# Kernel tuning notes

Hardware: AMD Instinct MI355X
Metric: run time of the kernel (lower is better)

The kernel has to match this reference:

```python
import jax, jax.numpy as jnp
import numpy as np

T, H, E, K, I, S = 512, 1024, 32, 4, 512, 2048  # tokens, hidden, experts, top_k, moe_inter, shared_inter


def setup_inputs() -> dict:
    key = jax.random.key(0)
    ks = jax.random.split(key, 8)
    sc = 0.02
    return {
        "hidden_states": jax.random.normal(ks[0], (T, H), jnp.float32),
        "Wg": jax.random.normal(ks[1], (H, E + 1), jnp.float32) * sc,          # router gate + shared gate (merged)
        "W_gate": jax.random.normal(ks[2], (E, H, I), jnp.float32) * sc,        # per-expert gate proj
        "W_up": jax.random.normal(ks[3], (E, H, I), jnp.float32) * sc,          # per-expert up proj
        "W_down": jax.random.normal(ks[4], (E, I, H), jnp.float32) * sc,        # per-expert down proj
        "Ws_gate": jax.random.normal(ks[5], (H, S), jnp.float32) * sc,          # shared expert gate proj
        "Ws_up": jax.random.normal(ks[6], (H, S), jnp.float32) * sc,            # shared expert up proj
        "Ws_down": jax.random.normal(ks[7], (S, H), jnp.float32) * sc,          # shared expert down proj
    }


def reference(hidden_states, Wg, W_gate, W_up, W_down, Ws_gate, Ws_up, Ws_down):
    x = hidden_states  # [T, H]
    logits = x @ Wg                       # [T, E+1]
    router_logits = logits[:, :E]         # [T, E]
    shared_gate_logits = logits[:, E:]    # [T, 1]

    # top-k softmax routing with renormalization (renormalize=True)
    probs = jax.nn.softmax(router_logits, axis=-1)          # [T, E]
    topk_w, topk_idx = jax.lax.top_k(probs, K)               # [T, K]
    topk_w = topk_w / jnp.sum(topk_w, axis=-1, keepdims=True)
    combine = jnp.zeros((T, E), x.dtype).at[jnp.arange(T)[:, None], topk_idx].add(topk_w)  # [T, E]

    # routed experts: dense reference over all experts, combined by routing weights
    g = jnp.einsum("th,ehi->eti", x, W_gate)                 # [E, T, I]
    u = jnp.einsum("th,ehi->eti", x, W_up)                   # [E, T, I]
    h = jax.nn.silu(g) * u                                    # SiluAndMul
    y = jnp.einsum("eti,eih->eth", h, W_down)                # [E, T, H]
    routed = jnp.einsum("te,eth->th", combine, y)            # [T, H]

    # shared expert MLP + sigmoid shared-gate
    sh = (jax.nn.silu(x @ Ws_gate) * (x @ Ws_up)) @ Ws_down  # [T, H]
    shared = jax.nn.sigmoid(shared_gate_logits) * sh

    return shared + routed
```

## Files before the change

### kernel.cpp

```cpp
#include <hip/hip_runtime.h>
#include <hip/hip_bf16.h>

#define TT 512
#define HH 1024
#define EE 32
#define KK 4
#define II 512
#define SS 2048

using f32x4 = __attribute__((ext_vector_type(4))) float;
using s16x8 = __attribute__((ext_vector_type(8))) short;

__device__ __forceinline__ unsigned short f2bf(float f){
  unsigned int u = __builtin_bit_cast(unsigned int, f);
  u += 0x7fffu + ((u >> 16) & 1u);
  return (unsigned short)(u >> 16);
}

__global__ __launch_bounds__(64) void k_router(
    const float* __restrict__ x, const float* __restrict__ Wg,
    unsigned short* __restrict__ xb, int* __restrict__ topk_idx,
    float* __restrict__ topk_w, float* __restrict__ sig_gate){
  int t = blockIdx.x; int l = threadIdx.x;
  const float* xr = x + (size_t)t * HH;
  #pragma unroll
  for(int i=0;i<HH/64;i++){
    int h = l + 64*i;
    xb[(size_t)t*HH + h] = f2bf(xr[h]);
  }
  float acc0=0.f, acc1=0.f, acc2=0.f, acc3=0.f;
  if(l < EE+1){
    const float* wcol = Wg + l;
    for(int h=0; h<HH; h+=4){
      acc0 += xr[h]   * wcol[(size_t)h*(EE+1)];
      acc1 += xr[h+1] * wcol[(size_t)(h+1)*(EE+1)];
      acc2 += xr[h+2] * wcol[(size_t)(h+2)*(EE+1)];
      acc3 += xr[h+3] * wcol[(size_t)(h+3)*(EE+1)];
    }
  }
  __shared__ float lg[EE+1];
  if(l < EE+1) lg[l] = (acc0+acc1)+(acc2+acc3);
  __syncthreads();
  if(l == 0){
    float v[EE];
    #pragma unroll
    for(int i=0;i<EE;i++) v[i]=lg[i];
    int idx[KK]; float val[KK];
    #pragma unroll
    for(int k=0;k<KK;k++){
      float m=-1e30f; int mi=0;
      for(int i=0;i<EE;i++){ if(v[i]>m){ m=v[i]; mi=i; } }
      idx[k]=mi; val[k]=m; v[mi]=-1e30f;
    }
    float mx = val[0], s=0.f; float w[KK];
    #pragma unroll
    for(int k=0;k<KK;k++){ w[k]=__expf(val[k]-mx); s+=w[k]; }
    float inv = 1.f/s;
    #pragma unroll
    for(int k=0;k<KK;k++){ topk_idx[t*KK+k]=idx[k]; topk_w[t*KK+k]=w[k]*inv; }
    sig_gate[t] = 1.f/(1.f+__expf(-lg[EE]));
  }
}

__global__ __launch_bounds__(64) void k_build(
    const int* __restrict__ topk_idx, const float* __restrict__ topk_w,
    int* __restrict__ token_list, float* __restrict__ weight_list,
    int* __restrict__ counts){
  int e = blockIdx.x; int l = threadIdx.x;
  int cnt = 0;
  for(int c=0;c<TT;c+=64){
    int t = c + l;
    int kk = -1;
    #pragma unroll
    for(int k=0;k<KK;k++) if(topk_idx[t*KK+k]==e) kk=k;
    unsigned long long b = __ballot(kk>=0);
    int pre = __popcll(b & ((1ull<<l)-1ull));
    if(kk>=0){
      token_list[e*TT + cnt + pre] = t;
      weight_list[e*TT + cnt + pre] = topk_w[t*KK+kk];
    }
    cnt += __popcll(b);
  }
  if(l==0) counts[e]=cnt;
}

__device__ __forceinline__ void stB(unsigned short* B, int nb, int krow,
                                    float4 r0, float4 r1){
  const float* a = (const float*)&r0;
  const float* b = (const float*)&r1;
  #pragma unroll
  for(int j=0;j<4;j++){
    unsigned v = (unsigned)f2bf(a[j]) | ((unsigned)f2bf(b[j]) << 16);
    *reinterpret_cast<unsigned*>(B + (size_t)(nb+j)*40 + krow) = v;
  }
}

template<bool DUAL>
__device__ __forceinline__ void gemm64(
    const unsigned short* A0, bool va,
    const float* Gp, const float* Up, int ldb, int NK,
    f32x4* ag, f32x4* au,
    unsigned short* As, unsigned short* Bg, unsigned short* Bu, int tid){
  const int w = tid>>6, l = tid&63;
  const int ar = tid>>2, as_ = tid&3;
  const int krow = 2*(tid>>4), nb = 4*(tid&15);
  const int kt = l>>4, mm = l&15;
  uint4 av = va ? *reinterpret_cast<const uint4*>(A0) : make_uint4(0,0,0,0);
  float4 g0 = *reinterpret_cast<const float4*>(Gp + (size_t)krow*ldb);
  float4 g1 = *reinterpret_cast<const float4*>(Gp + (size_t)(krow+1)*ldb);
  float4 u0, u1;
  if(DUAL){
    u0 = *reinterpret_cast<const float4*>(Up + (size_t)krow*ldb);
    u1 = *reinterpret_cast<const float4*>(Up + (size_t)(krow+1)*ldb);
  }
  *reinterpret_cast<uint4*>(As + (size_t)ar*40 + as_*8) = av;
  stB(Bg, nb, krow, g0, g1);
  if(DUAL) stB(Bu, nb, krow, u0, u1);
  __syncthreads();
  for(int ks=0; ks<NK; ks++){
    const int cur = ks & 1;
    const bool more = (ks+1 < NK);
    if(more){
      av = va ? *reinterpret_cast<const uint4*>(A0 + (size_t)(ks+1)*32)
              : make_uint4(0,0,0,0);
      const float* gb = Gp + (size_t)(ks+1)*32*ldb;
      g0 = *reinterpret_cast<const float4*>(gb + (size_t)krow*ldb);
      g1 = *reinterpret_cast<const float4*>(gb + (size_t)(krow+1)*ldb);
      if(DUAL){
        const float* ub = Up + (size_t)(ks+1)*32*ldb;
        u0 = *reinterpret_cast<const float4*>(ub + (size_t)krow*ldb);
        u1 = *reinterpret_cast<const float4*>(ub + (size_t)(krow+1)*ldb);
      }
    }
    s16x8 bg_[4], bu_[4];
    #pragma unroll
    for(int c=0;c<4;c++){
      bg_[c] = *reinterpret_cast<const s16x8*>(Bg + ((size_t)cur*64 + c*16 + mm)*40 + kt*8);
      if(DUAL)
        bu_[c] = *reinterpret_cast<const s16x8*>(Bu + ((size_t)cur*64 + c*16 + mm)*40 + kt*8);
    }
    s16x8 af = *reinterpret_cast<const s16x8*>(As + ((size_t)cur*64 + w*16 + mm)*40 + kt*8);
    #pragma unroll
    for(int c=0;c<4;c++){
      ag[c] = __builtin_amdgcn_mfma_f32_16x16x32_bf16(af, bg_[c], ag[c], 0,0,0);
      if(DUAL)
        au[c] = __builtin_amdgcn_mfma_f32_16x16x32_bf16(af, bu_[c], au[c], 0,0,0);
    }
    if(more){
      const int nx = cur^1;
      *reinterpret_cast<uint4*>(As + ((size_t)nx*64 + ar)*40 + as_*8) = av;
      stB(Bg + (size_t)nx*64*40, nb, krow, g0, g1);
      if(DUAL) stB(Bu + (size_t)nx*64*40, nb, krow, u0, u1);
    }
    __syncthreads();
  }
}

__global__ __launch_bounds__(256) void k_gateup_all(
    const unsigned short* __restrict__ xb,
    const float* __restrict__ Wsg, const float* __restrict__ Wsu,
    unsigned short* __restrict__ Hs,
    const float* __restrict__ Wgate, const float* __restrict__ Wup,
    const int* __restrict__ token_list, const int* __restrict__ counts,
    unsigned short* __restrict__ hbuf){
  __shared__ unsigned short As[2*64*40];
  __shared__ unsigned short Bg[2*64*40];
  __shared__ unsigned short Bu[2*64*40];
  int tid = threadIdx.x, w = tid>>6, l = tid&63;
  int ar = tid>>2, as_ = tid&3, nb = 4*(tid&15);
  int bid = blockIdx.x;
  f32x4 zero = {0.f,0.f,0.f,0.f};
  const int NSH = (TT/64)*(SS/64);

  if(bid < NSH){
    int n0 = (bid & 31) * 64;
    int r0 = (bid >> 5) * 64;
    f32x4 ag[4]={zero,zero,zero,zero}, au[4]={zero,zero,zero,zero};
    const unsigned short* A0 = xb + (size_t)(r0+ar)*HH + as_*8;
    const float* Gp = Wsg + n0 + nb;
    const float* Up = Wsu + n0 + nb;
    gemm64<true>(A0, true, Gp, Up, SS, HH/32, ag, au, As, Bg, Bu, tid);
    int mm = l&15, rb = r0 + w*16 + (l>>4)*4;
    #pragma unroll
    for(int c=0;c<4;c++){
      #pragma unroll
      for(int j=0;j<4;j++){
        float g = ag[c][j], u = au[c][j];
        Hs[(size_t)(rb+j)*SS + n0 + c*16 + mm] = f2bf(g*u/(1.f+__expf(-g)));
      }
    }
  } else {
    int b = bid - NSH;
    int e = b >> 3;
    int i0 = (b & 7) * 64;
    int cnt = counts[e]; if(cnt == 0) return;
    int off = 0;
    for(int i=0;i<e;i++) off += counts[i];
    const float* Gp0 = Wgate + (size_t)e*HH*II + i0 + nb;
    const float* Up0 = Wup   + (size_t)e*HH*II + i0 + nb;
    for(int rt=0; rt*64<cnt; rt++){
      int nv = cnt - rt*64; if(nv > 64) nv = 64;
      const int* rows = token_list + e*TT + rt*64;
      int arow = (ar < nv) ? rows[ar] : 0;
      bool va = ar < nv;
      f32x4 ag[4]={zero,zero,zero,zero}, au[4]={zero,zero,zero,zero};
      const unsigned short* A0 = xb + (size_t)arow*HH + as_*8;
      gemm64<true>(A0, va, Gp0, Up0, II, HH/32, ag, au, As, Bg, Bu, tid);
      int mm = l&15, rr0 = w*16 + (l>>4)*4;
      #pragma unroll
      for(int c=0;c<4;c++){
        #pragma unroll
        for(int j=0;j<4;j++){
          int rr = rr0 + j;
          if(rr < nv){
            float g = ag[c][j], u = au[c][j];
            hbuf[(size_t)(off+rt*64+rr)*II + i0 + c*16 + mm] =
                f2bf(g*u/(1.f+__expf(-g)));
          }
        }
      }
    }
  }
}

__global__ __launch_bounds__(256) void k_down_all(
    const unsigned short* __restrict__ Hsrc, const float* __restrict__ Wsd,
    const float* __restrict__ sig_gate,
    const unsigned short* __restrict__ hbuf, const float* __restrict__ Wdown,
    const int* __restrict__ token_list, const float* __restrict__ weight_list,
    const int* __restrict__ counts, float* __restrict__ out){
  __shared__ unsigned short As[2*64*40];
  __shared__ unsigned short Bs[2*64*40];
  int tid = threadIdx.x, w = tid>>6, l = tid&63;
  int ar = tid>>2, as_ = tid&3, nb = 4*(tid&15);
  int bid = blockIdx.x;
  f32x4 zero = {0.f,0.f,0.f,0.f};
  const int NSH = (TT/64)*(HH/64);

  if(bid < NSH){
    int n0 = (bid & 15) * 64;
    int r0 = (bid >> 4) * 64;
    f32x4 acc[4]={zero,zero,zero,zero};
    const unsigned short* A0 = Hsrc + (size_t)(r0+ar)*SS + as_*8;
    const float* Bp = Wsd + n0 + nb;
    gemm64<false>(A0, true, Bp, Bp, HH, SS/32, acc, acc, As, Bs, Bs, tid);
    int mm = l&15, rb = r0 + w*16 + (l>>4)*4;
    #pragma unroll
    for(int c=0;c<4;c++){
      #pragma unroll
      for(int j=0;j<4;j++){
        atomicAdd(&out[(size_t)(rb+j)*HH + n0 + c*16 + mm],
                  sig_gate[rb+j]*acc[c][j]);
      }
    }
  } else {
    int b = bid - NSH;
    int e = b >> 4;
    int n0 = (b & 15) * 64;
    int cnt = counts[e]; if(cnt == 0) return;
    int off = 0;
    for(int i=0;i<e;i++) off += counts[i];
    const float* Bp = Wdown + (size_t)e*II*HH + n0 + nb;
    for(int rt=0; rt*64<cnt; rt++){
      int nv = cnt - rt*64; if(nv > 64) nv = 64;
      bool va = ar < nv;
      f32x4 acc[4]={zero,zero,zero,zero};
      const unsigned short* A0 = hbuf + (size_t)(off+rt*64+ar)*II + as_*8;
      gemm64<false>(A0, va, Bp, Bp, HH, II/32, acc, acc, As, Bs, Bs, tid);
      int mm = l&15, rr0 = w*16 + (l>>4)*4;
      #pragma unroll
      for(int c=0;c<4;c++){
        #pragma unroll
        for(int j=0;j<4;j++){
          int rr = rr0 + j;
          if(rr < nv){
            int t = token_list[e*TT + rt*64 + rr];
            float wt = weight_list[e*TT + rt*64 + rr];
            atomicAdd(&out[(size_t)t*HH + n0 + c*16 + mm], wt*acc[c][j]);
          }
        }
      }
    }
  }
}

extern "C" void kernel_launch(void* const* d_in, const int* in_sizes, int n_in,
                              void* d_out, int out_size, void* d_ws, size_t ws_size,
                              hipStream_t stream) {
  const float* x     = (const float*)d_in[0];
  const float* Wg    = (const float*)d_in[1];
  const float* Wgate = (const float*)d_in[2];
  const float* Wup   = (const float*)d_in[3];
  const float* Wdown = (const float*)d_in[4];
  const float* Wsg   = (const float*)d_in[5];
  const float* Wsu   = (const float*)d_in[6];
  const float* Wsd   = (const float*)d_in[7];
  float* out = (float*)d_out;

  char* ws = (char*)d_ws;
  unsigned short* xb   = (unsigned short*)ws; ws += (size_t)TT*HH*2;
  unsigned short* Hs   = (unsigned short*)ws; ws += (size_t)TT*SS*2;
  unsigned short* hbuf = (unsigned short*)ws; ws += (size_t)(TT*KK+64)*II*2;
  int*   token_list  = (int*)ws;   ws += (size_t)EE*TT*4;
  float* weight_list = (float*)ws; ws += (size_t)EE*TT*4;
  int*   topk_idx    = (int*)ws;   ws += (size_t)TT*KK*4;
  float* topk_wq     = (float*)ws; ws += (size_t)TT*KK*4;
  int*   counts      = (int*)ws;   ws += 128;
  float* sig_gate    = (float*)ws; ws += (size_t)TT*4;

  hipMemsetAsync(d_out, 0, (size_t)TT*HH*4, stream);
  k_router<<<TT, 64, 0, stream>>>(x, Wg, xb, topk_idx, topk_wq, sig_gate);
  k_build<<<EE, 64, 0, stream>>>(topk_idx, topk_wq, token_list, weight_list, counts);
  k_gateup_all<<<(TT/64)*(SS/64) + EE*(II/64), 256, 0, stream>>>(
      xb, Wsg, Wsu, Hs, Wgate, Wup, token_list, counts, hbuf);
  k_down_all<<<(TT/64)*(HH/64) + EE*(HH/64), 256, 0, stream>>>(
      Hs, Wsd, sig_gate, hbuf, Wdown, token_list, weight_list, counts, out);
}
```

Baseline: 151.9 us.

## Restructure MFMA GEMM tile with swizzled packed-B LDS layout and two-deep prefetch

Rewrites the shared 64x64 GEMM helper so that B tiles are stored as packed bf16 pairs in an XOR-swizzled 32-bit layout. Each thread now writes one 16-byte vector store instead of four scattered 4-byte stores, which is meant to reduce LDS bank conflicts on the transpose-on-store. The k-loop is unrolled by two, with global loads issued two stages ahead in two register sets, so global latency is hidden better. __syncthreads is replaced by an lgkmcnt wait plus s_barrier. The cost is higher register pressure, and the B fragments are now read with four scalar LDS reads each.

```diff
diff --git a/kernel.cpp b/kernel.cpp
--- a/kernel.cpp
+++ b/kernel.cpp
@@ -10,11 +10,19 @@
 
 using f32x4 = __attribute__((ext_vector_type(4))) float;
 using s16x8 = __attribute__((ext_vector_type(8))) short;
+using u32x4 = __attribute__((ext_vector_type(4))) unsigned;
 
 __device__ __forceinline__ unsigned short f2bf(float f){
   unsigned int u = __builtin_bit_cast(unsigned int, f);
   u += 0x7fffu + ((u >> 16) & 1u);
   return (unsigned short)(u >> 16);
+}
+__device__ __forceinline__ unsigned pk2(float a, float b){
+  return (unsigned)f2bf(a) | ((unsigned)f2bf(b) << 16);
+}
+__device__ __forceinline__ void barrier_lds(){
+  asm volatile("s_waitcnt lgkmcnt(0)" ::: "memory");
+  __builtin_amdgcn_s_barrier();
 }
 
 __global__ __launch_bounds__(64) void k_router(
@@ -84,75 +92,86 @@
   if(l==0) counts[e]=cnt;
 }
 
-__device__ __forceinline__ void stB(unsigned short* B, int nb, int krow,
-                                    float4 r0, float4 r1){
-  const float* a = (const float*)&r0;
-  const float* b = (const float*)&r1;
-  #pragma unroll
-  for(int j=0;j<4;j++){
-    unsigned v = (unsigned)f2bf(a[j]) | ((unsigned)f2bf(b[j]) << 16);
-    *reinterpret_cast<unsigned*>(B + (size_t)(nb+j)*40 + krow) = v;
-  }
-}
-
 template<bool DUAL>
 __device__ __forceinline__ void gemm64(
-    const unsigned short* A0, bool va,
-    const float* Gp, const float* Up, int ldb, int NK,
+    const unsigned short* __restrict__ A0, bool va,
+    const float* __restrict__ Gp, const float* __restrict__ Up,
+    int ldb, int NK,
     f32x4* ag, f32x4* au,
-    unsigned short* As, unsigned short* Bg, unsigned short* Bu, int tid){
+    unsigned short* As, unsigned* Bg, unsigned* Bu, int tid){
   const int w = tid>>6, l = tid&63;
   const int ar = tid>>2, as_ = tid&3;
-  const int krow = 2*(tid>>4), nb = 4*(tid&15);
+  const int m16 = tid&15, g2 = tid>>4;
+  const int krow = 2*g2;
   const int kt = l>>4, mm = l&15;
-  uint4 av = va ? *reinterpret_cast<const uint4*>(A0) : make_uint4(0,0,0,0);
-  float4 g0 = *reinterpret_cast<const float4*>(Gp + (size_t)krow*ldb);
-  float4 g1 = *reinterpret_cast<const float4*>(Gp + (size_t)(krow+1)*ldb);
-  float4 u0, u1;
-  if(DUAL){
-    u0 = *reinterpret_cast<const float4*>(Up + (size_t)krow*ldb);
-    u1 = *reinterpret_cast<const float4*>(Up + (size_t)(krow+1)*ldb);
-  }
-  *reinterpret_cast<uint4*>(As + (size_t)ar*40 + as_*8) = av;
-  stB(Bg, nb, krow, g0, g1);
-  if(DUAL) stB(Bu, nb, krow, u0, u1);
-  __syncthreads();
-  for(int ks=0; ks<NK; ks++){
-    const int cur = ks & 1;
-    const bool more = (ks+1 < NK);
-    if(more){
-      av = va ? *reinterpret_cast<const uint4*>(A0 + (size_t)(ks+1)*32)
-              : make_uint4(0,0,0,0);
-      const float* gb = Gp + (size_t)(ks+1)*32*ldb;
-      g0 = *reinterpret_cast<const float4*>(gb + (size_t)krow*ldb);
-      g1 = *reinterpret_cast<const float4*>(gb + (size_t)(krow+1)*ldb);
+  const unsigned swW = ((unsigned)((g2>>2)&3))<<3;
+  const int wB  = g2*64 + ((4*m16) ^ (int)swW);
+  const int aWr = ar*40 + as_*8;
+  const int aRd = (w*16+mm)*40 + kt*8;
+  const unsigned swR = ((unsigned)(kt&3))<<3;
+
+  uint4 avA, avB;
+  float4 gA0,gA1,uA0,uA1, gB0,gB1,uB0,uB1;
+
+  auto loadBatch = [&](int b, uint4& av, float4& g0, float4& g1,
+                       float4& u0, float4& u1){
+    av = va ? *reinterpret_cast<const uint4*>(A0 + (size_t)b*32)
+            : make_uint4(0,0,0,0);
+    const float* p = Gp + (size_t)(b*32 + krow)*ldb;
+    g0 = *reinterpret_cast<const float4*>(p);
+    g1 = *reinterpret_cast<const float4*>(p + ldb);
+    if(DUAL){
+      const float* q = Up + (size_t)(b*32 + krow)*ldb;
+      u0 = *reinterpret_cast<const float4*>(q);
+      u1 = *reinterpret_cast<const float4*>(q + ldb);
+    }
+  };
+  auto storeBatch = [&](int h, uint4 av, float4 g0, float4 g1,
+                        float4 u0, float4 u1){
+    *reinterpret_cast<uint4*>(As + (size_t)h*64*40 + aWr) = av;
+    u32x4 vg; vg.x=pk2(g0.x,g1.x); vg.y=pk2(g0.y,g1.y);
+    vg.z=pk2(g0.z,g1.z); vg.w=pk2(g0.w,g1.w);
+    *reinterpret_cast<u32x4*>(Bg + (size_t)h*16*64 + wB) = vg;
+    if(DUAL){
+      u32x4 vu; vu.x=pk2(u0.x,u1.x); vu.y=pk2(u0.y,u1.y);
+      vu.z=pk2(u0.z,u1.z); vu.w=pk2(u0.w,u1.w);
+      *reinterpret_cast<u32x4*>(Bu + (size_t)h*16*64 + wB) = vu;
+    }
+  };
+  auto compute = [&](int h){
+    const unsigned* Bgh = Bg + (size_t)h*16*64;
+    const unsigned* Buh = Bu + (size_t)h*16*64;
+    s16x8 af = *reinterpret_cast<const s16x8*>(As + (size_t)h*64*40 + aRd);
+    #pragma unroll
+    for(int c=0;c<4;c++){
+      int base = kt*4*64 + (((c*16+mm)) ^ (int)swR);
+      u32x4 tg; tg.x=Bgh[base]; tg.y=Bgh[base+64];
+      tg.z=Bgh[base+128]; tg.w=Bgh[base+192];
+      s16x8 bg_ = __builtin_bit_cast(s16x8, tg);
+      ag[c] = __builtin_amdgcn_mfma_f32_16x16x32_bf16(af, bg_, ag[c], 0,0,0);
       if(DUAL){
-        const float* ub = Up + (size_t)(ks+1)*32*ldb;
-        u0 = *reinterpret_cast<const float4*>(ub + (size_t)krow*ldb);
-        u1 = *reinterpret_cast<const float4*>(ub + (size_t)(krow+1)*ldb);
-      }
-    }
-    s16x8 bg_[4], bu_[4];
-    #pragma unroll
-    for(int c=0;c<4;c++){
-      bg_[c] = *reinterpret_cast<const s16x8*>(Bg + ((size_t)cur*64 + c*16 + mm)*40 + kt*8);
-      if(DUAL)
-        bu_[c] = *reinterpret_cast<const s16x8*>(Bu + ((size_t)cur*64 + c*16 + mm)*40 + kt*8);
-    }
-    s16x8 af = *reinterpret_cast<const s16x8*>(As + ((size_t)cur*64 + w*16 + mm)*40 + kt*8);
-    #pragma unroll
-    for(int c=0;c<4;c++){
-      ag[c] = __builtin_amdgcn_mfma_f32_16x16x32_bf16(af, bg_[c], ag[c], 0,0,0);
-      if(DUAL)
-        au[c] = __builtin_amdgcn_mfma_f32_16x16x32_bf16(af, bu_[c], au[c], 0,0,0);
-    }
-    if(more){
-      const int nx = cur^1;
-      *reinterpret_cast<uint4*>(As + ((size_t)nx*64 + ar)*40 + as_*8) = av;
-      stB(Bg + (size_t)nx*64*40, nb, krow, g0, g1);
-      if(DUAL) stB(Bu + (size_t)nx*64*40, nb, krow, u0, u1);
-    }
-    __syncthreads();
+        u32x4 tu; tu.x=Buh[base]; tu.y=Buh[base+64];
+        tu.z=Buh[base+128]; tu.w=Buh[base+192];
+        s16x8 bu_ = __builtin_bit_cast(s16x8, tu);
+        au[c] = __builtin_amdgcn_mfma_f32_16x16x32_bf16(af, bu_, au[c], 0,0,0);
+      }
+    }
+  };
+
+  loadBatch(0, avA, gA0,gA1, uA0,uA1);
+  loadBatch(1, avB, gB0,gB1, uB0,uB1);
+  storeBatch(0, avA, gA0,gA1, uA0,uA1);
+  barrier_lds();
+  for(int ks=0; ks<NK; ks+=2){
+    const bool m2 = (ks+2 < NK), m3 = (ks+3 < NK);
+    if(m2) loadBatch(ks+2, avA, gA0,gA1, uA0,uA1);
+    compute(0);
+    storeBatch(1, avB, gB0,gB1, uB0,uB1);
+    barrier_lds();
+    if(m3) loadBatch(ks+3, avB, gB0,gB1, uB0,uB1);
+    compute(1);
+    if(m2) storeBatch(0, avA, gA0,gA1, uA0,uA1);
+    barrier_lds();
   }
 }
 
@@ -163,11 +182,11 @@
     const float* __restrict__ Wgate, const float* __restrict__ Wup,
     const int* __restrict__ token_list, const int* __restrict__ counts,
     unsigned short* __restrict__ hbuf){
-  __shared__ unsigned short As[2*64*40];
-  __shared__ unsigned short Bg[2*64*40];
-  __shared__ unsigned short Bu[2*64*40];
+  __shared__ __align__(16) unsigned short As[2*64*40];
+  __shared__ __align__(16) unsigned Bg[2*16*64];
+  __shared__ __align__(16) unsigned Bu[2*16*64];
   int tid = threadIdx.x, w = tid>>6, l = tid&63;
-  int ar = tid>>2, as_ = tid&3, nb = 4*(tid&15);
+  int ar = tid>>2, as_ = tid&3, m16 = tid&15;
   int bid = blockIdx.x;
   f32x4 zero = {0.f,0.f,0.f,0.f};
   const int NSH = (TT/64)*(SS/64);
@@ -177,8 +196,8 @@
     int r0 = (bid >> 5) * 64;
     f32x4 ag[4]={zero,zero,zero,zero}, au[4]={zero,zero,zero,zero};
     const unsigned short* A0 = xb + (size_t)(r0+ar)*HH + as_*8;
-    const float* Gp = Wsg + n0 + nb;
-    const float* Up = Wsu + n0 + nb;
+    const float* Gp = Wsg + n0 + 4*m16;
+    const float* Up = Wsu + n0 + 4*m16;
     gemm64<true>(A0, true, Gp, Up, SS, HH/32, ag, au, As, Bg, Bu, tid);
     int mm = l&15, rb = r0 + w*16 + (l>>4)*4;
     #pragma unroll
@@ -196,8 +215,8 @@
     int cnt = counts[e]; if(cnt == 0) return;
     int off = 0;
     for(int i=0;i<e;i++) off += counts[i];
-    const float* Gp0 = Wgate + (size_t)e*HH*II + i0 + nb;
-    const float* Up0 = Wup   + (size_t)e*HH*II + i0 + nb;
+    const float* Gp0 = Wgate + (size_t)e*HH*II + i0 + 4*m16;
+    const float* Up0 = Wup   + (size_t)e*HH*II + i0 + 4*m16;
     for(int rt=0; rt*64<cnt; rt++){
       int nv = cnt - rt*64; if(nv > 64) nv = 64;
       const int* rows = token_list + e*TT + rt*64;
@@ -229,10 +248,10 @@
     const unsigned short* __restrict__ hbuf, const float* __restrict__ Wdown,
     const int* __restrict__ token_list, const float* __restrict__ weight_list,
     const int* __restrict__ counts, float* __restrict__ out){
-  __shared__ unsigned short As[2*64*40];
-  __shared__ unsigned short Bs[2*64*40];
+  __shared__ __align__(16) unsigned short As[2*64*40];
+  __shared__ __align__(16) unsigned Bs[2*16*64];
   int tid = threadIdx.x, w = tid>>6, l = tid&63;
-  int ar = tid>>2, as_ = tid&3, nb = 4*(tid&15);
+  int ar = tid>>2, as_ = tid&3, m16 = tid&15;
   int bid = blockIdx.x;
   f32x4 zero = {0.f,0.f,0.f,0.f};
   const int NSH = (TT/64)*(HH/64);
@@ -242,7 +261,7 @@
     int r0 = (bid >> 4) * 64;
     f32x4 acc[4]={zero,zero,zero,zero};
     const unsigned short* A0 = Hsrc + (size_t)(r0+ar)*SS + as_*8;
-    const float* Bp = Wsd + n0 + nb;
+    const float* Bp = Wsd + n0 + 4*m16;
     gemm64<false>(A0, true, Bp, Bp, HH, SS/32, acc, acc, As, Bs, Bs, tid);
     int mm = l&15, rb = r0 + w*16 + (l>>4)*4;
     #pragma unroll
@@ -260,7 +279,7 @@
     int cnt = counts[e]; if(cnt == 0) return;
     int off = 0;
     for(int i=0;i<e;i++) off += counts[i];
-    const float* Bp = Wdown + (size_t)e*II*HH + n0 + nb;
+    const float* Bp = Wdown + (size_t)e*II*HH + n0 + 4*m16;
     for(int rt=0; rt*64<cnt; rt++){
       int nv = cnt - rt*64; if(nv > 64) nv = 64;
       bool va = ar < nv;
```

Result: no change. 151.2 us (-0.5%).

## Pre-convert weights to packed bf16 MFMA layout and drop LDS staging

Applied to the files above, without the earlier changes.

Adds a conversion kernel that turns every fp32 weight matrix into bf16 packed in k-groups of 8, so each lane can load its MFMA B-fragment straight from global memory. The GEMM loop loses its shared-memory staging and barriers and instead keeps register double buffers for A and B. A small scan kernel now computes per-expert offsets once instead of every block summing the counts. The trade is an extra full pass over all weights each call (read fp32, write bf16, read bf16 again), and each B row is now loaded by several waves with no reuse through LDS.

```diff
diff --git a/kernel.cpp b/kernel.cpp
--- a/kernel.cpp
+++ b/kernel.cpp
@@ -84,90 +84,93 @@
   if(l==0) counts[e]=cnt;
 }
 
-__device__ __forceinline__ void stB(unsigned short* B, int nb, int krow,
-                                    float4 r0, float4 r1){
-  const float* a = (const float*)&r0;
-  const float* b = (const float*)&r1;
+__global__ __launch_bounds__(64) void k_scan(
+    const int* __restrict__ counts, int* __restrict__ offs){
+  if(threadIdx.x==0){
+    int o=0;
+    for(int e=0;e<EE;e++){ offs[e]=o; o+=counts[e]; }
+  }
+}
+
+__global__ __launch_bounds__(256) void k_convert(
+    const float* __restrict__ src, unsigned short* __restrict__ dst,
+    int K, int N){
+  int nm = blockIdx.z;
+  const float* S = src + (size_t)nm*K*N;
+  unsigned short* D = dst + (size_t)nm*K*N;
+  int k0 = blockIdx.y*8, n0 = blockIdx.x*256;
+  __shared__ float tile[8][260];
+  int t = threadIdx.x;
+  int row = t>>5, c8 = (t&31)*8;
+  const float* p = S + (size_t)(k0+row)*N + n0 + c8;
+  float4 v0 = *reinterpret_cast<const float4*>(p);
+  float4 v1 = *reinterpret_cast<const float4*>(p+4);
+  *reinterpret_cast<float4*>(&tile[row][c8])   = v0;
+  *reinterpret_cast<float4*>(&tile[row][c8+4]) = v1;
+  __syncthreads();
+  unsigned short u[8];
   #pragma unroll
-  for(int j=0;j<4;j++){
-    unsigned v = (unsigned)f2bf(a[j]) | ((unsigned)f2bf(b[j]) << 16);
-    *reinterpret_cast<unsigned*>(B + (size_t)(nb+j)*40 + krow) = v;
-  }
-}
+  for(int r=0;r<8;r++) u[r] = f2bf(tile[r][t]);
+  uint4 o;
+  o.x = (unsigned)u[0] | ((unsigned)u[1]<<16);
+  o.y = (unsigned)u[2] | ((unsigned)u[3]<<16);
+  o.z = (unsigned)u[4] | ((unsigned)u[5]<<16);
+  o.w = (unsigned)u[6] | ((unsigned)u[7]<<16);
+  *reinterpret_cast<uint4*>(D + ((size_t)(k0>>3)*N + n0 + t)*8) = o;
+}
+
+
+#define LD16(p) (*reinterpret_cast<const uint4*>(p))
+__device__ __forceinline__ s16x8 cvt16(uint4 v){ return __builtin_bit_cast(s16x8, v); }
 
 template<bool DUAL>
-__device__ __forceinline__ void gemm64(
-    const unsigned short* A0, bool va,
-    const float* Gp, const float* Up, int ldb, int NK,
-    f32x4* ag, f32x4* au,
-    unsigned short* As, unsigned short* Bg, unsigned short* Bu, int tid){
-  const int w = tid>>6, l = tid&63;
-  const int ar = tid>>2, as_ = tid&3;
-  const int krow = 2*(tid>>4), nb = 4*(tid&15);
-  const int kt = l>>4, mm = l&15;
-  uint4 av = va ? *reinterpret_cast<const uint4*>(A0) : make_uint4(0,0,0,0);
-  float4 g0 = *reinterpret_cast<const float4*>(Gp + (size_t)krow*ldb);
-  float4 g1 = *reinterpret_cast<const float4*>(Gp + (size_t)(krow+1)*ldb);
-  float4 u0, u1;
-  if(DUAL){
-    u0 = *reinterpret_cast<const float4*>(Up + (size_t)krow*ldb);
-    u1 = *reinterpret_cast<const float4*>(Up + (size_t)(krow+1)*ldb);
-  }
-  *reinterpret_cast<uint4*>(As + (size_t)ar*40 + as_*8) = av;
-  stB(Bg, nb, krow, g0, g1);
-  if(DUAL) stB(Bu, nb, krow, u0, u1);
-  __syncthreads();
+__device__ __forceinline__ void gemm_rd(
+    const unsigned short* __restrict__ Ap,
+    const unsigned short* __restrict__ Gp,
+    const unsigned short* __restrict__ Up,
+    int N, int NK, f32x4* ag, f32x4* au){
+  uint4 a0, g0[4], u0[4], a1, g1[4], u1[4];
+  a0 = LD16(Ap);
+  #pragma unroll
+  for(int c=0;c<4;c++){
+    g0[c] = LD16(Gp + c*128);
+    if(DUAL) u0[c] = LD16(Up + c*128);
+  }
   for(int ks=0; ks<NK; ks++){
-    const int cur = ks & 1;
     const bool more = (ks+1 < NK);
     if(more){
-      av = va ? *reinterpret_cast<const uint4*>(A0 + (size_t)(ks+1)*32)
-              : make_uint4(0,0,0,0);
-      const float* gb = Gp + (size_t)(ks+1)*32*ldb;
-      g0 = *reinterpret_cast<const float4*>(gb + (size_t)krow*ldb);
-      g1 = *reinterpret_cast<const float4*>(gb + (size_t)(krow+1)*ldb);
+      a1 = LD16(Ap + (size_t)(ks+1)*32);
+      const unsigned short* gp = Gp + (size_t)(ks+1)*32*N;
+      #pragma unroll
+      for(int c=0;c<4;c++) g1[c] = LD16(gp + c*128);
       if(DUAL){
-        const float* ub = Up + (size_t)(ks+1)*32*ldb;
-        u0 = *reinterpret_cast<const float4*>(ub + (size_t)krow*ldb);
-        u1 = *reinterpret_cast<const float4*>(ub + (size_t)(krow+1)*ldb);
-      }
-    }
-    s16x8 bg_[4], bu_[4];
+        const unsigned short* up = Up + (size_t)(ks+1)*32*N;
+        #pragma unroll
+        for(int c=0;c<4;c++) u1[c] = LD16(up + c*128);
+      }
+    }
+    s16x8 af = cvt16(a0);
     #pragma unroll
     for(int c=0;c<4;c++){
-      bg_[c] = *reinterpret_cast<const s16x8*>(Bg + ((size_t)cur*64 + c*16 + mm)*40 + kt*8);
+      ag[c] = __builtin_amdgcn_mfma_f32_16x16x32_bf16(af, cvt16(g0[c]), ag[c], 0,0,0);
       if(DUAL)
-        bu_[c] = *reinterpret_cast<const s16x8*>(Bu + ((size_t)cur*64 + c*16 + mm)*40 + kt*8);
-    }
-    s16x8 af = *reinterpret_cast<const s16x8*>(As + ((size_t)cur*64 + w*16 + mm)*40 + kt*8);
-    #pragma unroll
-    for(int c=0;c<4;c++){
-      ag[c] = __builtin_amdgcn_mfma_f32_16x16x32_bf16(af, bg_[c], ag[c], 0,0,0);
-      if(DUAL)
-        au[c] = __builtin_amdgcn_mfma_f32_16x16x32_bf16(af, bu_[c], au[c], 0,0,0);
-    }
-    if(more){
-      const int nx = cur^1;
-      *reinterpret_cast<uint4*>(As + ((size_t)nx*64 + ar)*40 + as_*8) = av;
-      stB(Bg + (size_t)nx*64*40, nb, krow, g0, g1);
-      if(DUAL) stB(Bu + (size_t)nx*64*40, nb, krow, u0, u1);
-    }
-    __syncthreads();
-  }
-}
-
-__global__ __launch_bounds__(256) void k_gateup_all(
+        au[c] = __builtin_amdgcn_mfma_f32_16x16x32_bf16(af, cvt16(u0[c]), au[c], 0,0,0);
+    }
+    a0 = a1;
+    #pragma unroll
+    for(int c=0;c<4;c++){ g0[c]=g1[c]; if(DUAL) u0[c]=u1[c]; }
+  }
+}
+
+__global__ __launch_bounds__(256) void k_gateup(
     const unsigned short* __restrict__ xb,
-    const float* __restrict__ Wsg, const float* __restrict__ Wsu,
+    const unsigned short* __restrict__ Bsg, const unsigned short* __restrict__ Bsu,
     unsigned short* __restrict__ Hs,
-    const float* __restrict__ Wgate, const float* __restrict__ Wup,
+    const unsigned short* __restrict__ Bgate, const unsigned short* __restrict__ Bup,
     const int* __restrict__ token_list, const int* __restrict__ counts,
-    unsigned short* __restrict__ hbuf){
-  __shared__ unsigned short As[2*64*40];
-  __shared__ unsigned short Bg[2*64*40];
-  __shared__ unsigned short Bu[2*64*40];
+    const int* __restrict__ offs, unsigned short* __restrict__ hbuf){
   int tid = threadIdx.x, w = tid>>6, l = tid&63;
-  int ar = tid>>2, as_ = tid&3, nb = 4*(tid&15);
+  int n16 = l&15, q = l>>4;
   int bid = blockIdx.x;
   f32x4 zero = {0.f,0.f,0.f,0.f};
   const int NSH = (TT/64)*(SS/64);
@@ -176,17 +179,17 @@
     int n0 = (bid & 31) * 64;
     int r0 = (bid >> 5) * 64;
     f32x4 ag[4]={zero,zero,zero,zero}, au[4]={zero,zero,zero,zero};
-    const unsigned short* A0 = xb + (size_t)(r0+ar)*HH + as_*8;
-    const float* Gp = Wsg + n0 + nb;
-    const float* Up = Wsu + n0 + nb;
-    gemm64<true>(A0, true, Gp, Up, SS, HH/32, ag, au, As, Bg, Bu, tid);
-    int mm = l&15, rb = r0 + w*16 + (l>>4)*4;
+    const unsigned short* Ap = xb + (size_t)(r0 + w*16 + n16)*HH + q*8;
+    const unsigned short* Gp = Bsg + ((size_t)q*SS + n0 + n16)*8;
+    const unsigned short* Up = Bsu + ((size_t)q*SS + n0 + n16)*8;
+    gemm_rd<true>(Ap, Gp, Up, SS, HH/32, ag, au);
+    int rb = r0 + w*16 + q*4;
     #pragma unroll
     for(int c=0;c<4;c++){
       #pragma unroll
       for(int j=0;j<4;j++){
         float g = ag[c][j], u = au[c][j];
-        Hs[(size_t)(rb+j)*SS + n0 + c*16 + mm] = f2bf(g*u/(1.f+__expf(-g)));
+        Hs[(size_t)(rb+j)*SS + n0 + c*16 + n16] = f2bf(g*u/(1.f+__expf(-g)));
       }
     }
   } else {
@@ -194,19 +197,17 @@
     int e = b >> 3;
     int i0 = (b & 7) * 64;
     int cnt = counts[e]; if(cnt == 0) return;
-    int off = 0;
-    for(int i=0;i<e;i++) off += counts[i];
-    const float* Gp0 = Wgate + (size_t)e*HH*II + i0 + nb;
-    const float* Up0 = Wup   + (size_t)e*HH*II + i0 + nb;
+    int off = offs[e];
+    const unsigned short* Gb = Bgate + (size_t)e*HH*II + ((size_t)q*II + i0 + n16)*8;
+    const unsigned short* Ub = Bup   + (size_t)e*HH*II + ((size_t)q*II + i0 + n16)*8;
     for(int rt=0; rt*64<cnt; rt++){
       int nv = cnt - rt*64; if(nv > 64) nv = 64;
-      const int* rows = token_list + e*TT + rt*64;
-      int arow = (ar < nv) ? rows[ar] : 0;
-      bool va = ar < nv;
+      int ra = w*16 + n16; if(ra >= nv) ra = nv-1;
+      int rowA = token_list[e*TT + rt*64 + ra];
       f32x4 ag[4]={zero,zero,zero,zero}, au[4]={zero,zero,zero,zero};
-      const unsigned short* A0 = xb + (size_t)arow*HH + as_*8;
-      gemm64<true>(A0, va, Gp0, Up0, II, HH/32, ag, au, As, Bg, Bu, tid);
-      int mm = l&15, rr0 = w*16 + (l>>4)*4;
+      const unsigned short* Ap = xb + (size_t)rowA*HH + q*8;
+      gemm_rd<true>(Ap, Gb, Ub, II, HH/32, ag, au);
+      int rr0 = w*16 + q*4;
       #pragma unroll
       for(int c=0;c<4;c++){
         #pragma unroll
@@ -214,7 +215,7 @@
           int rr = rr0 + j;
           if(rr < nv){
             float g = ag[c][j], u = au[c][j];
-            hbuf[(size_t)(off+rt*64+rr)*II + i0 + c*16 + mm] =
+            hbuf[(size_t)(off+rt*64+rr)*II + i0 + c*16 + n16] =
                 f2bf(g*u/(1.f+__expf(-g)));
           }
         }
@@ -223,16 +224,15 @@
   }
 }
 
-__global__ __launch_bounds__(256) void k_down_all(
-    const unsigned short* __restrict__ Hsrc, const float* __restrict__ Wsd,
+__global__ __launch_bounds__(256) void k_down(
+    const unsigned short* __restrict__ Hsrc, const unsigned short* __restrict__ Bsd,
     const float* __restrict__ sig_gate,
-    const unsigned short* __restrict__ hbuf, const float* __restrict__ Wdown,
+    const unsigned short* __restrict__ hbuf, const unsigned short* __restrict__ Bdown,
     const int* __restrict__ token_list, const float* __restrict__ weight_list,
-    const int* __restrict__ counts, float* __restrict__ out){
-  __shared__ unsigned short As[2*64*40];
-  __shared__ unsigned short Bs[2*64*40];
+    const int* __restrict__ counts, const int* __restrict__ offs,
+    float* __restrict__ out){
   int tid = threadIdx.x, w = tid>>6, l = tid&63;
-  int ar = tid>>2, as_ = tid&3, nb = 4*(tid&15);
+  int n16 = l&15, q = l>>4;
   int bid = blockIdx.x;
   f32x4 zero = {0.f,0.f,0.f,0.f};
   const int NSH = (TT/64)*(HH/64);
@@ -241,15 +241,15 @@
     int n0 = (bid & 15) * 64;
     int r0 = (bid >> 4) * 64;
     f32x4 acc[4]={zero,zero,zero,zero};
-    const unsigned short* A0 = Hsrc + (size_t)(r0+ar)*SS + as_*8;
-    const float* Bp = Wsd + n0 + nb;
-    gemm64<false>(A0, true, Bp, Bp, HH, SS/32, acc, acc, As, Bs, Bs, tid);
-    int mm = l&15, rb = r0 + w*16 + (l>>4)*4;
+    const unsigned short* Ap = Hsrc + (size_t)(r0 + w*16 + n16)*SS + q*8;
+    const unsigned short* Bp = Bsd + ((size_t)q*HH + n0 + n16)*8;
+    gemm_rd<false>(Ap, Bp, Bp, HH, SS/32, acc, acc);
+    int rb = r0 + w*16 + q*4;
     #pragma unroll
     for(int c=0;c<4;c++){
       #pragma unroll
       for(int j=0;j<4;j++){
-        atomicAdd(&out[(size_t)(rb+j)*HH + n0 + c*16 + mm],
+        atomicAdd(&out[(size_t)(rb+j)*HH + n0 + c*16 + n16],
                   sig_gate[rb+j]*acc[c][j]);
       }
     }
@@ -258,16 +258,15 @@
     int e = b >> 4;
     int n0 = (b & 15) * 64;
     int cnt = counts[e]; if(cnt == 0) return;
-    int off = 0;
-    for(int i=0;i<e;i++) off += counts[i];
-    const float* Bp = Wdown + (size_t)e*II*HH + n0 + nb;
+    int off = offs[e];
+    const unsigned short* Bb = Bdown + (size_t)e*II*HH + ((size_t)q*HH + n0 + n16)*8;
     for(int rt=0; rt*64<cnt; rt++){
       int nv = cnt - rt*64; if(nv > 64) nv = 64;
-      bool va = ar < nv;
+      int ra = w*16 + n16; if(ra >= nv) ra = nv-1;
       f32x4 acc[4]={zero,zero,zero,zero};
-      const unsigned short* A0 = hbuf + (size_t)(off+rt*64+ar)*II + as_*8;
-      gemm64<false>(A0, va, Bp, Bp, HH, II/32, acc, acc, As, Bs, Bs, tid);
-      int mm = l&15, rr0 = w*16 + (l>>4)*4;
+      const unsigned short* Ap = hbuf + (size_t)(off+rt*64+ra)*II + q*8;
+      gemm_rd<false>(Ap, Bb, Bb, HH, II/32, acc, acc);
+      int rr0 = w*16 + q*4;
       #pragma unroll
       for(int c=0;c<4;c++){
         #pragma unroll
@@ -276,7 +275,7 @@
           if(rr < nv){
             int t = token_list[e*TT + rt*64 + rr];
             float wt = weight_list[e*TT + rt*64 + rr];
-            atomicAdd(&out[(size_t)t*HH + n0 + c*16 + mm], wt*acc[c][j]);
+            atomicAdd(&out[(size_t)t*HH + n0 + c*16 + n16], wt*acc[c][j]);
           }
         }
       }
@@ -306,13 +305,27 @@
   int*   topk_idx    = (int*)ws;   ws += (size_t)TT*KK*4;
   float* topk_wq     = (float*)ws; ws += (size_t)TT*KK*4;
   int*   counts      = (int*)ws;   ws += 128;
+  int*   offsb       = (int*)ws;   ws += 128;
   float* sig_gate    = (float*)ws; ws += (size_t)TT*4;
+  unsigned short* Bsg   = (unsigned short*)ws; ws += (size_t)HH*SS*2;
+  unsigned short* Bsu   = (unsigned short*)ws; ws += (size_t)HH*SS*2;
+  unsigned short* Bgate = (unsigned short*)ws; ws += (size_t)EE*HH*II*2;
+  unsigned short* Bup   = (unsigned short*)ws; ws += (size_t)EE*HH*II*2;
+  unsigned short* Bdown = (unsigned short*)ws; ws += (size_t)EE*II*HH*2;
+  unsigned short* Bsd   = (unsigned short*)ws; ws += (size_t)SS*HH*2;
 
   hipMemsetAsync(d_out, 0, (size_t)TT*HH*4, stream);
   k_router<<<TT, 64, 0, stream>>>(x, Wg, xb, topk_idx, topk_wq, sig_gate);
   k_build<<<EE, 64, 0, stream>>>(topk_idx, topk_wq, token_list, weight_list, counts);
-  k_gateup_all<<<(TT/64)*(SS/64) + EE*(II/64), 256, 0, stream>>>(
-      xb, Wsg, Wsu, Hs, Wgate, Wup, token_list, counts, hbuf);
-  k_down_all<<<(TT/64)*(HH/64) + EE*(HH/64), 256, 0, stream>>>(
-      Hs, Wsd, sig_gate, hbuf, Wdown, token_list, weight_list, counts, out);
-}
+  k_scan<<<1, 64, 0, stream>>>(counts, offsb);
+  k_convert<<<dim3(SS/256, HH/8, 1),  256, 0, stream>>>(Wsg, Bsg, HH, SS);
+  k_convert<<<dim3(SS/256, HH/8, 1),  256, 0, stream>>>(Wsu, Bsu, HH, SS);
+  k_convert<<<dim3(II/256, HH/8, EE), 256, 0, stream>>>(Wgate, Bgate, HH, II);
+  k_convert<<<dim3(II/256, HH/8, EE), 256, 0, stream>>>(Wup, Bup, HH, II);
+  k_gateup<<<(TT/64)*(SS/64) + EE*(II/64), 256, 0, stream>>>(
+      xb, Bsg, Bsu, Hs, Bgate, Bup, token_list, counts, offsb, hbuf);
+  k_convert<<<dim3(HH/256, II/8, EE), 256, 0, stream>>>(Wdown, Bdown, II, HH);
+  k_convert<<<dim3(HH/256, SS/8, 1),  256, 0, stream>>>(Wsd, Bsd, SS, HH);
+  k_down<<<(TT/64)*(HH/64) + EE*(HH/64), 256, 0, stream>>>(
+      Hs, Bsd, sig_gate, hbuf, Bdown, token_list, weight_list, counts, offsb, out);
+}
```

Measured after the change: 229.0 us. 1.51x slower.
